# Performance work log

Measured on AMD Instinct MI355X. Metric: run time of the kernel, lower is better.

Reference implementation:

```python
import jax, jax.numpy as jnp
import numpy as np

B, HC, WC, KC = 4, 32, 32, 1024   # coarse feature map (ResNet101 layer3)
HF, WF, KF = 128, 128, 256        # fine feature map (ResNet101 layer1)
DC = 4                            # downscale_coef; HF // DC == HC


def setup_inputs() -> dict:
    key = jax.random.key(0)
    k1, k2, k3, k4 = jax.random.split(key, 4)
    return {
        "F_g1_coarse": jax.random.normal(k1, (B, HC, WC, KC), jnp.float32),
        "F_gk_coarse": jax.random.normal(k2, (B, HC, WC, KC), jnp.float32),
        "F_g1_fine": jax.random.normal(k3, (B, HF, WF, KF), jnp.float32),
        "F_gk_fine": jax.random.normal(k4, (B, HF, WF, KF), jnp.float32),
    }


def _coarse_match(f1, fk):
    # For every coarse position in Gk find nearest (L2) coarse position in G1.
    b, h, w, k = f1.shape
    a = f1.reshape(b, h * w, k)   # G1 positions
    q = fk.reshape(b, h * w, k)   # Gk positions
    # ||q||^2 + ||a||^2 - 2 q.a  -> [B, HW_gk, HW_g1]
    d = ((q * q).sum(-1)[:, :, None]
         + (a * a).sum(-1)[:, None, :]
         - 2.0 * jnp.einsum('bnk,bmk->bnm', q, a))
    idx = jnp.argmin(d, axis=-1)                       # [B, HW]
    cm = jnp.stack([idx // w, idx % w], axis=-1)       # (row, col) in G1
    return cm.reshape(b, h, w, 2).astype(jnp.int32)


def _fine_match(f1, fk, cm, dc):
    # Refine each dc x dc fine tile of Gk by searching the fine pixels of G1
    # covered by the coarse matches of the 3x3 coarse-neighborhood.
    b, h, w, k = fk.shape
    hc, wc = h // dc, w // dc
    off = jnp.arange(-1, 2)
    nI = jnp.clip(jnp.arange(hc)[:, None] + off[None, :], 0, hc - 1)  # [Hc,3]
    nJ = jnp.clip(jnp.arange(wc)[:, None] + off[None, :], 0, wc - 1)  # [Wc,3]
    # neighbor coarse matches: [B, Hc, Wc, 3, 3, 2]
    nb = cm[:, nI[:, None, :, None], nJ[None, :, None, :]]
    nb = nb.reshape(b, hc, wc, 9, 2)
    # expand each coarse match to its dc*dc fine pixels in G1
    sr = jnp.repeat(jnp.arange(dc), dc)   # [dc^2] row shifts
    sc = jnp.tile(jnp.arange(dc), dc)     # [dc^2] col shifts
    ncand = 9 * dc * dc                   # 144 candidates per tile
    cand_r = (nb[..., 0][..., None] * dc + sr).reshape(b, hc, wc, ncand)
    cand_c = (nb[..., 1][..., None] * dc + sc).reshape(b, hc, wc, ncand)
    # gather candidate fine features from G1: [B, Hc, Wc, N, K]
    bi = jnp.arange(b)[:, None, None, None]
    cand_f = f1[bi, cand_r, cand_c]
    # fine tile features of Gk: [B, Hc, Wc, dc^2, K]
    fkb = fk.reshape(b, hc, dc, wc, dc, k).transpose(0, 1, 3, 2, 4, 5)
    fkb = fkb.reshape(b, hc, wc, dc * dc, k)
    dist = ((fkb * fkb).sum(-1)[..., :, None]
            + (cand_f * cand_f).sum(-1)[..., None, :]
            - 2.0 * jnp.einsum('bhwpk,bhwnk->bhwpn', fkb, cand_f))
    best = jnp.argmin(dist, axis=-1)      # [B, Hc, Wc, dc^2]
    hi = jnp.arange(hc)[None, :, None, None]
    wi = jnp.arange(wc)[None, None, :, None]
    best_r = cand_r[bi, hi, wi, best]     # [B, Hc, Wc, dc^2]
    best_c = cand_c[bi, hi, wi, best]
    def to_grid(x):
        return x.reshape(b, hc, wc, dc, dc).transpose(0, 1, 3, 2, 4).reshape(b, h, w)
    return jnp.stack([to_grid(best_r), to_grid(best_c)], axis=-1).astype(jnp.int32)


def reference(F_g1_coarse, F_gk_coarse, F_g1_fine, F_gk_fine):
    closest_coarse = _coarse_match(F_g1_coarse, F_gk_coarse)   # [B,Hc,Wc,2]
    closest_fine = _fine_match(F_g1_fine, F_gk_fine, closest_coarse, DC)  # [B,H,W,2]
    return closest_coarse, closest_fine
```

## Files before the change

### kernel.cpp

```cpp
#include <hip/hip_runtime.h>
#include <cstdint>
#include <cstddef>

#define BB 4
#define HCC 32
#define WCC 32
#define KCC 1024
#define NCC (HCC*WCC)
#define HFF 128
#define WFF 128
#define KFF 256
#define DCC 4
#define NCHUNK 8

typedef _Float16 half8 __attribute__((ext_vector_type(8)));
typedef _Float16 half4_t __attribute__((ext_vector_type(4)));
typedef float f32x4 __attribute__((ext_vector_type(4)));
#define MFMA16(a,b,c) __builtin_amdgcn_mfma_f32_16x16x32_f16((a),(b),(c),0,0,0)
#define INV2K 0.00048828125f

__device__ inline void cvt8(const float4 u0, const float4 u1, half8& h, half8& l2) {
  float uu[8];
  *(float4*)uu = u0; *(float4*)(uu + 4) = u1;
  #pragma unroll
  for (int e = 0; e < 8; ++e) {
    _Float16 hh = (_Float16)uu[e];
    float r = (uu[e] - (float)hh) * 2048.0f;
    h[e] = hh; l2[e] = (_Float16)r;
  }
}

template<int K>
__global__ __launch_bounds__(256) void preconv_kernel(
    const float* __restrict__ src0, const float* __restrict__ src1,
    _Float16* __restrict__ hi0, _Float16* __restrict__ lo0,
    _Float16* __restrict__ hi1, _Float16* __restrict__ lo1,
    float* __restrict__ nr0, float* __restrict__ nr1, int rows) {
  const float* __restrict__ src = blockIdx.y ? src1 : src0;
  _Float16* __restrict__ hi = blockIdx.y ? hi1 : hi0;
  _Float16* __restrict__ lo = blockIdx.y ? lo1 : lo0;
  float* __restrict__ nrm = blockIdx.y ? nr1 : nr0;
  const int wave = threadIdx.x >> 6, lane = threadIdx.x & 63;
  const int row = blockIdx.x * 4 + wave;
  if (row >= rows) return;
  const float* p = src + (size_t)row * K;
  const size_t ob = (size_t)row * K + lane * 4;
  float s = 0.f;
  #pragma unroll
  for (int c = 0; c < K / 256; ++c) {
    float4 v = *(const float4*)(p + c * 256 + lane * 4);
    s += v.x*v.x + v.y*v.y + v.z*v.z + v.w*v.w;
    float vv[4] = {v.x, v.y, v.z, v.w};
    half4_t h, l2;
    #pragma unroll
    for (int e = 0; e < 4; ++e) {
      _Float16 hh = (_Float16)vv[e];
      l2[e] = (_Float16)((vv[e] - (float)hh) * 2048.0f);
      h[e] = hh;
    }
    *(half4_t*)(hi + ob + c * 256) = h;
    *(half4_t*)(lo + ob + c * 256) = l2;
  }
  #pragma unroll
  for (int m = 1; m <= 32; m <<= 1) s += __shfl_xor(s, m, 64);
  if (lane == 0) nrm[row] = s;
}

__global__ __launch_bounds__(256) void preconv_fine_kernel(
    const float* __restrict__ src, _Float16* __restrict__ hl,
    float* __restrict__ nrm, int rows) {
  const int wave = threadIdx.x >> 6, lane = threadIdx.x & 63;
  const int row = blockIdx.x * 4 + wave;
  if (row >= rows) return;
  float4 v = *(const float4*)(src + (size_t)row * KFF + lane * 4);
  float s = v.x*v.x + v.y*v.y + v.z*v.z + v.w*v.w;
  float vv[4] = {v.x, v.y, v.z, v.w};
  half4_t h, l2;
  #pragma unroll
  for (int e = 0; e < 4; ++e) {
    _Float16 hh = (_Float16)vv[e];
    l2[e] = (_Float16)((vv[e] - (float)hh) * 2048.0f);
    h[e] = hh;
  }
  const size_t dst = (size_t)row * 512 + (lane >> 3) * 64 + ((lane >> 1) & 3) * 16 + (lane & 1) * 4;
  *(half4_t*)(hl + dst)     = h;
  *(half4_t*)(hl + dst + 8) = l2;
  #pragma unroll
  for (int m = 1; m <= 32; m <<= 1) s += __shfl_xor(s, m, 64);
  if (lane == 0) nrm[row] = s;
}

__global__ __launch_bounds__(256) void coarse_kernel3(
    const _Float16* __restrict__ gAhi, const _Float16* __restrict__ gAlo,
    const _Float16* __restrict__ gBhi, const _Float16* __restrict__ gBlo,
    const float* __restrict__ na, const float* __restrict__ nq,
    float* __restrict__ pval, int* __restrict__ pidx) {
  __shared__ _Float16 Ahi[128][64], Alo[128][64];
  __shared__ _Float16 Bhi[64][64],  Blo[64][64];
  __shared__ float a2s[128], q2s[64];
  __shared__ float redv[2][64];
  __shared__ int   redi[2][64];

  const int t = threadIdx.x;
  const int chunk = blockIdx.x;
  const int n0 = blockIdx.y * 64;
  const int b  = blockIdx.z;
  const int m0 = chunk * 128;

  const int ar = t >> 1, ahf = t & 1;
  const int brw = t >> 2, bq = t & 3;
  const int l  = t & 63;
  const int wv = t >> 6;
  const int wm = wv >> 1, wn = wv & 1;

  if (t < 128) a2s[t] = na[b*NCC + m0 + t];
  else if (t < 192) q2s[t - 128] = nq[b*NCC + n0 + (t - 128)];

  const _Float16* __restrict__ gah = gAhi + (size_t)(b*NCC + m0 + ar) * KCC + ahf * 32;
  const _Float16* __restrict__ gal = gAlo + (size_t)(b*NCC + m0 + ar) * KCC + ahf * 32;
  const _Float16* __restrict__ gbh = gBhi + (size_t)(b*NCC + n0 + brw) * KCC + bq * 16;
  const _Float16* __restrict__ gbl = gBlo + (size_t)(b*NCC + n0 + brw) * KCC + bq * 16;

  f32x4 accA[4][2], accB[4][2];
  #pragma unroll
  for (int mt = 0; mt < 4; ++mt)
    #pragma unroll
    for (int nt = 0; nt < 2; ++nt) { accA[mt][nt] = (f32x4)0.f; accB[mt][nt] = (f32x4)0.f; }

  half8 pah[4], pal[4], pbh[2], pbl[2];
  #pragma unroll
  for (int c2 = 0; c2 < 4; ++c2) { pah[c2] = *(const half8*)(gah + c2*8); pal[c2] = *(const half8*)(gal + c2*8); }
  #pragma unroll
  for (int c2 = 0; c2 < 2; ++c2) { pbh[c2] = *(const half8*)(gbh + c2*8); pbl[c2] = *(const half8*)(gbl + c2*8); }

  for (int k0 = 0; k0 < KCC; k0 += 64) {
    __syncthreads();
    #pragma unroll
    for (int c2 = 0; c2 < 4; ++c2) {
      int cs = (ahf * 4 + c2) ^ (ar & 7);
      *(half8*)&Ahi[ar][cs * 8] = pah[c2];
      *(half8*)&Alo[ar][cs * 8] = pal[c2];
    }
    #pragma unroll
    for (int c2 = 0; c2 < 2; ++c2) {
      int cs = (bq * 2 + c2) ^ (brw & 7);
      *(half8*)&Bhi[brw][cs * 8] = pbh[c2];
      *(half8*)&Blo[brw][cs * 8] = pbl[c2];
    }
    __syncthreads();

    if (k0 + 64 < KCC) {
      #pragma unroll
      for (int c2 = 0; c2 < 4; ++c2) {
        pah[c2] = *(const half8*)(gah + k0 + 64 + c2*8);
        pal[c2] = *(const half8*)(gal + k0 + 64 + c2*8);
      }
      #pragma unroll
      for (int c2 = 0; c2 < 2; ++c2) {
        pbh[c2] = *(const half8*)(gbh + k0 + 64 + c2*8);
        pbl[c2] = *(const half8*)(gbl + k0 + 64 + c2*8);
      }
    }

    #pragma unroll
    for (int kk = 0; kk < 2; ++kk) {
      const int cs = ((kk * 4 + (l >> 4)) ^ (l & 7)) * 8;
      half8 ah[4], al[4], bh[2], bl[2];
      #pragma unroll
      for (int mt = 0; mt < 4; ++mt) {
        int row = wm * 64 + mt * 16 + (l & 15);
        ah[mt] = *(const half8*)&Ahi[row][cs];
        al[mt] = *(const half8*)&Alo[row][cs];
      }
      #pragma unroll
      for (int nt = 0; nt < 2; ++nt) {
        int row = wn * 32 + nt * 16 + (l & 15);
        bh[nt] = *(const half8*)&Bhi[row][cs];
        bl[nt] = *(const half8*)&Blo[row][cs];
      }
      #pragma unroll
      for (int mt = 0; mt < 4; ++mt)
        #pragma unroll
        for (int nt = 0; nt < 2; ++nt) {
          accA[mt][nt] = MFMA16(ah[mt], bh[nt], accA[mt][nt]);
          accB[mt][nt] = MFMA16(ah[mt], bl[nt], accB[mt][nt]);
          accB[mt][nt] = MFMA16(al[mt], bh[nt], accB[mt][nt]);
        }
    }
  }

  #pragma unroll
  for (int nt = 0; nt < 2; ++nt) {
    float q2 = q2s[wn * 32 + nt * 16 + (l & 15)];
    float bv = 3.0e38f; int bi = 0;
    #pragma unroll
    for (int mt = 0; mt < 4; ++mt)
      #pragma unroll
      for (int r = 0; r < 4; ++r) {
        float dot = accA[mt][nt][r] + accB[mt][nt][r] * INV2K;
        int ml = wm * 64 + mt * 16 + (l >> 4) * 4 + r;
        float d = (q2 + a2s[ml]) - 2.0f * dot;
        if (d < bv) { bv = d; bi = m0 + ml; }
      }
    #pragma unroll
    for (int mm = 16; mm < 64; mm <<= 1) {
      float ov = __shfl_xor(bv, mm, 64);
      int oi = __shfl_xor(bi, mm, 64);
      if (ov < bv || (ov == bv && oi < bi)) { bv = ov; bi = oi; }
    }
    if ((l >> 4) == 0) { redv[wm][wn*32 + nt*16 + l] = bv; redi[wm][wn*32 + nt*16 + l] = bi; }
  }
  __syncthreads();
  if (t < 64) {
    float v0 = redv[0][t]; int i0 = redi[0][t];
    float v1 = redv[1][t]; int i1 = redi[1][t];
    if (v1 < v0) { v0 = v1; i0 = i1; }
    pval[((size_t)b * NCC + n0 + t) * NCHUNK + chunk] = v0;
    pidx[((size_t)b * NCC + n0 + t) * NCHUNK + chunk] = i0;
  }
}

__global__ __launch_bounds__(256) void coarse_reduce_kernel(
    const float* __restrict__ pval, const int* __restrict__ pidx,
    int* __restrict__ out) {
  int g = blockIdx.x * 256 + threadIdx.x;
  if (g >= BB * NCC) return;
  float bv = pval[(size_t)g * NCHUNK];
  int bi = pidx[(size_t)g * NCHUNK];
  #pragma unroll
  for (int c = 1; c < NCHUNK; ++c) {
    float v = pval[(size_t)g * NCHUNK + c];
    int ix = pidx[(size_t)g * NCHUNK + c];
    if (v < bv) { bv = v; bi = ix; }
  }
  out[(size_t)g*2]     = bi >> 5;
  out[(size_t)g*2 + 1] = bi & 31;
}

__global__ __launch_bounds__(512, 2) void fine_kernel6(
    const _Float16* __restrict__ gHL, const float* __restrict__ fkf,
    const float* __restrict__ naf, const int* __restrict__ coarse,
    int* __restrict__ outf) {
  __shared__ _Float16 CS[2][384 * 64];
  __shared__ int   rIdx[384];
  __shared__ float tNORM[384];
  __shared__ int cbr[24], cbc[24];
  __shared__ float redv[8][16];
  __shared__ int   redi[8][16];

  const int t = threadIdx.x;
  const int bx = blockIdx.x, by = blockIdx.y, b = blockIdx.z;
  const int l = t & 63, w = t >> 6;
  const int cy = w >> 2, cx = w & 3;
  const int ii = by * 2 + cy, jj = bx * 4 + cx;

  if (t < 24) {
    int wy = t / 6, wx = t % 6;
    int y = min(max(by * 2 - 1 + wy, 0), HCC - 1);
    int x = min(max(bx * 4 - 1 + wx, 0), WCC - 1);
    int base = ((b * HCC + y) * WCC + x) * 2;
    cbr[t] = coarse[base]; cbc[t] = coarse[base + 1];
  }
  __syncthreads();
  if (t < 384) {
    int slot = t >> 4, s = t & 15;
    int row = cbr[slot] * DCC + (s >> 2), col = cbc[slot] * DCC + (s & 3);
    int g = (b * HFF + row) * WFF + col;
    rIdx[t] = g; tNORM[t] = naf[g];
  }
  __syncthreads();

  unsigned srcOff[6], dstOff[6];
  #pragma unroll
  for (int it = 0; it < 6; ++it) {
    int g2 = it * 512 + t;
    int rowG = g2 >> 3, lc = g2 & 7;
    srcOff[it] = (unsigned)rIdx[rowG] * 512u + (unsigned)((lc >> 1) * 16 + (lc & 1) * 8);
    dstOff[it] = (unsigned)(rowG * 64 + (lc ^ (rowG & 7)) * 8);
  }

  const int q = l >> 4, r = l & 15;
  const int qfr = ii * DCC + (r >> 2), qfc = jj * DCC + (r & 3);
  const float* qsrc = fkf + ((size_t)(b * HFF + qfr) * WFF + qfc) * KFF + q * 8;

  half8 pf[6];
  #pragma unroll
  for (int it = 0; it < 6; ++it) pf[it] = *(const half8*)(gHL + srcOff[it]);
  #pragma unroll
  for (int it = 0; it < 6; ++it) *(half8*)&CS[0][dstOff[it]] = pf[it];
  #pragma unroll
  for (int it = 0; it < 6; ++it) pf[it] = *(const half8*)(gHL + srcOff[it] + 64u);
  float4 qu0 = *(const float4*)(qsrc);
  float4 qu1 = *(const float4*)(qsrc + 4);
  __syncthreads();

  f32x4 accA[9], accB[9];
  #pragma unroll
  for (int T = 0; T < 9; ++T) { accA[T] = (f32x4)0.f; accB[T] = (f32x4)0.f; }

  const int woff[9] = {0, 1, 2, 6, 7, 8, 12, 13, 14};
  const int wbase = cy * 6 + cx;
  const int rsw = r & 7;
  const int c0 = ((q * 2) ^ rsw) * 8, c1 = ((q * 2 + 1) ^ rsw) * 8;
  float qnp = 0.f;

  #pragma unroll
  for (int ke = 0; ke < 8; ++ke) {
    const int cur = ke & 1;
    qnp += qu0.x*qu0.x + qu0.y*qu0.y + qu0.z*qu0.z + qu0.w*qu0.w
         + qu1.x*qu1.x + qu1.y*qu1.y + qu1.z*qu1.z + qu1.w*qu1.w;
    half8 bh, bl;
    cvt8(qu0, qu1, bh, bl);
    if (ke < 7) {
      qu0 = *(const float4*)(qsrc + (ke + 1) * 32);
      qu1 = *(const float4*)(qsrc + (ke + 1) * 32 + 4);
    }
    #pragma unroll
    for (int T = 0; T < 9; ++T) {
      int rowG = (wbase + woff[T]) * 16 + r;
      half8 ah = *(const half8*)&CS[cur][rowG * 64 + c0];
      half8 al = *(const half8*)&CS[cur][rowG * 64 + c1];
      accA[T] = MFMA16(ah, bh, accA[T]);
      accB[T] = MFMA16(ah, bl, accB[T]);
      accB[T] = MFMA16(al, bh, accB[T]);
    }
    if (ke < 7) {
      #pragma unroll
      for (int it = 0; it < 6; ++it) *(half8*)&CS[cur ^ 1][dstOff[it]] = pf[it];
      if (ke < 6) {
        #pragma unroll
        for (int it = 0; it < 6; ++it)
          pf[it] = *(const half8*)(gHL + srcOff[it] + (unsigned)(ke + 2) * 64u);
      }
    }
    __syncthreads();
  }

  qnp += __shfl_xor(qnp, 16, 64);
  qnp += __shfl_xor(qnp, 32, 64);
  const float q2v = qnp;

  {
    float bv = 3.0e38f; int bi = 0;
    #pragma unroll
    for (int T = 0; T < 9; ++T) {
      int slot = wbase + woff[T];
      #pragma unroll
      for (int r2 = 0; r2 < 4; ++r2) {
        int s4 = q * 4 + r2;
        float cn = tNORM[slot * 16 + s4];
        float dot = accA[T][r2] + accB[T][r2] * INV2K;
        float d = (q2v + cn) - 2.0f * dot;
        int m = T * 16 + s4;
        if (d < bv) { bv = d; bi = m; }
      }
    }
    #pragma unroll
    for (int mm = 16; mm < 64; mm <<= 1) {
      float ov = __shfl_xor(bv, mm, 64);
      int oi = __shfl_xor(bi, mm, 64);
      if (ov < bv || (ov == bv && oi < bi)) { bv = ov; bi = oi; }
    }
    if (l < 16) {
      int T = bi >> 4, s3 = bi & 15, slot = wbase + woff[T];
      int br = cbr[slot] * DCC + (s3 >> 2);
      int bc = cbc[slot] * DCC + (s3 & 3);
      int fr = ii * DCC + (l >> 2), fc = jj * DCC + (l & 3);
      size_t ob = ((size_t)(b * HFF + fr) * WFF + fc) * 2;
      outf[ob]     = br;
      outf[ob + 1] = bc;
    }
  }
  (void)redv; (void)redi;
}

__global__ __launch_bounds__(256, 2) void coarse_kernel(
    const float* __restrict__ f1, const float* __restrict__ fk,
    float* __restrict__ pval, int* __restrict__ pidx) {
  __shared__ _Float16 Ahi[128][64], Alo[128][64];
  __shared__ _Float16 Bhi[64][64],  Blo[64][64];
  __shared__ float npA[256], npB[256];
  __shared__ float a2s[128], q2s[64];
  __shared__ float redv[2][64];
  __shared__ int   redi[2][64];

  const int t = threadIdx.x;
  const int chunk = blockIdx.x;
  const int n0 = blockIdx.y * 64;
  const int b  = blockIdx.z;
  const int m0 = chunk * 128;

  const float* __restrict__ Abase = f1 + ((size_t)b * NCC + m0) * KCC;
  const float* __restrict__ Bbase = fk + ((size_t)b * NCC + n0) * KCC;

  const int ar = t >> 1, ahf = t & 1;
  const int brw = t >> 2, bq = t & 3;
  const int l  = t & 63;
  const int wv = t >> 6;
  const int wm = wv >> 1, wn = wv & 1;

  float nrmA = 0.f, nrmB = 0.f;
  f32x4 accA[4][2], accB[4][2];
  #pragma unroll
  for (int mt = 0; mt < 4; ++mt)
    #pragma unroll
    for (int nt = 0; nt < 2; ++nt) { accA[mt][nt] = (f32x4)0.f; accB[mt][nt] = (f32x4)0.f; }

  for (int k0 = 0; k0 < KCC; k0 += 64) {
    __syncthreads();
    {
      const float4* src = (const float4*)(Abase + (size_t)ar * KCC + k0 + ahf * 32);
      float4 va[8];
      #pragma unroll
      for (int i2 = 0; i2 < 8; ++i2) va[i2] = src[i2];
      #pragma unroll
      for (int i2 = 0; i2 < 8; ++i2)
        nrmA += va[i2].x*va[i2].x + va[i2].y*va[i2].y + va[i2].z*va[i2].z + va[i2].w*va[i2].w;
      #pragma unroll
      for (int c2 = 0; c2 < 4; ++c2) {
        half8 hh, hl;
        cvt8(va[c2*2], va[c2*2+1], hh, hl);
        int cs = (ahf * 4 + c2) ^ (ar & 7);
        *(half8*)&Ahi[ar][cs * 8] = hh;
        *(half8*)&Alo[ar][cs * 8] = hl;
      }
    }
    {
      const float4* src = (const float4*)(Bbase + (size_t)brw * KCC + k0 + bq * 16);
      float4 vb[4];
      #pragma unroll
      for (int i2 = 0; i2 < 4; ++i2) vb[i2] = src[i2];
      #pragma unroll
      for (int i2 = 0; i2 < 4; ++i2)
        nrmB += vb[i2].x*vb[i2].x + vb[i2].y*vb[i2].y + vb[i2].z*vb[i2].z + vb[i2].w*vb[i2].w;
      #pragma unroll
      for (int c2 = 0; c2 < 2; ++c2) {
        half8 hh, hl;
        cvt8(vb[c2*2], vb[c2*2+1], hh, hl);
        int cs = (bq * 2 + c2) ^ (brw & 7);
        *(half8*)&Bhi[brw][cs * 8] = hh;
        *(half8*)&Blo[brw][cs * 8] = hl;
      }
    }
    __syncthreads();

    #pragma unroll
    for (int kk = 0; kk < 2; ++kk) {
      const int cs = ((kk * 4 + (l >> 4)) ^ (l & 7)) * 8;
      half8 ah[4], al[4], bh[2], bl[2];
      #pragma unroll
      for (int mt = 0; mt < 4; ++mt) {
        int row = wm * 64 + mt * 16 + (l & 15);
        ah[mt] = *(const half8*)&Ahi[row][cs];
        al[mt] = *(const half8*)&Alo[row][cs];
      }
      #pragma unroll
      for (int nt = 0; nt < 2; ++nt) {
        int row = wn * 32 + nt * 16 + (l & 15);
        bh[nt] = *(const half8*)&Bhi[row][cs];
        bl[nt] = *(const half8*)&Blo[row][cs];
      }
      #pragma unroll
      for (int mt = 0; mt < 4; ++mt)
        #pragma unroll
        for (int nt = 0; nt < 2; ++nt) {
          accA[mt][nt] = MFMA16(ah[mt], bh[nt], accA[mt][nt]);
          accB[mt][nt] = MFMA16(ah[mt], bl[nt], accB[mt][nt]);
          accB[mt][nt] = MFMA16(al[mt], bh[nt], accB[mt][nt]);
        }
    }
  }

  npA[t] = nrmA; npB[t] = nrmB;
  __syncthreads();
  if (t < 128) a2s[t] = npA[2*t] + npA[2*t + 1];
  if (t < 64)  q2s[t] = npB[4*t] + npB[4*t + 1] + npB[4*t + 2] + npB[4*t + 3];
  __syncthreads();

  #pragma unroll
  for (int nt = 0; nt < 2; ++nt) {
    float q2 = q2s[wn * 32 + nt * 16 + (l & 15)];
    float bv = 3.0e38f; int bi = 0;
    #pragma unroll
    for (int mt = 0; mt < 4; ++mt)
      #pragma unroll
      for (int r = 0; r < 4; ++r) {
        float dot = accA[mt][nt][r] + accB[mt][nt][r] * INV2K;
        int ml = wm * 64 + mt * 16 + (l >> 4) * 4 + r;
        float d = (q2 + a2s[ml]) - 2.0f * dot;
        if (d < bv) { bv = d; bi = m0 + ml; }
      }
    #pragma unroll
    for (int mm = 16; mm < 64; mm <<= 1) {
      float ov = __shfl_xor(bv, mm, 64);
      int oi = __shfl_xor(bi, mm, 64);
      if (ov < bv || (ov == bv && oi < bi)) { bv = ov; bi = oi; }
    }
    if ((l >> 4) == 0) { redv[wm][wn*32 + nt*16 + l] = bv; redi[wm][wn*32 + nt*16 + l] = bi; }
  }
  __syncthreads();
  if (t < 64) {
    float v0 = redv[0][t]; int i0 = redi[0][t];
    float v1 = redv[1][t]; int i1 = redi[1][t];
    if (v1 < v0) { v0 = v1; i0 = i1; }
    pval[((size_t)b * NCC + n0 + t) * NCHUNK + chunk] = v0;
    pidx[((size_t)b * NCC + n0 + t) * NCHUNK + chunk] = i0;
  }
}

__global__ __launch_bounds__(192) void fine_kernel(
    const float* __restrict__ f1, const float* __restrict__ fkf,
    const int* __restrict__ coarse, int* __restrict__ outf) {
  __shared__ _Float16 Qhi[16][256], Qlo[16][256];
  __shared__ float qn[16], cn[144];
  __shared__ int cROW[144];
  __shared__ int cbr[9], cbc[9];
  __shared__ float redv[3][16];
  __shared__ int   redi[3][16];

  const int t = threadIdx.x;
  const int j = blockIdx.x, i = blockIdx.y, b = blockIdx.z;
  const int l = t & 63, wv = t >> 6;

  if (t < 9) {
    int di = t / 3 - 1, dj = t % 3 - 1;
    int y = min(max(i + di, 0), HCC - 1);
    int x = min(max(j + dj, 0), WCC - 1);
    int base = ((b*HCC + y)*WCC + x) * 2;
    cbr[t] = coarse[base];
    cbc[t] = coarse[base + 1];
  }
  __syncthreads();
  if (t < 144) {
    int n9 = t >> 4, s = t & 15;
    int row = cbr[n9]*DCC + (s >> 2), col = cbc[n9]*DCC + (s & 3);
    cROW[t] = (b*HFF + row)*WFF + col;
  }
  if (t < 64) {
    int qr = l & 15, qq = l >> 4;
    int fr = i*DCC + (qr >> 2), fc = j*DCC + (qr & 3);
    const float* src = fkf + ((size_t)(b*HFF + fr)*WFF + fc) * KFF + qq * 64;
    float s2 = 0.f;
    #pragma unroll
    for (int c2 = 0; c2 < 8; ++c2) {
      float4 u0 = *(const float4*)(src + c2*8);
      float4 u1 = *(const float4*)(src + c2*8 + 4);
      s2 += u0.x*u0.x + u0.y*u0.y + u0.z*u0.z + u0.w*u0.w
          + u1.x*u1.x + u1.y*u1.y + u1.z*u1.z + u1.w*u1.w;
      half8 hh, hl;
      cvt8(u0, u1, hh, hl);
      int cs = (qq * 8 + c2) ^ (qr & 7);
      *(half8*)&Qhi[qr][cs * 8] = hh;
      *(half8*)&Qlo[qr][cs * 8] = hl;
    }
    s2 += __shfl_xor(s2, 16, 64);
    s2 += __shfl_xor(s2, 32, 64);
    if (qq == 0) qn[qr] = s2;
  }
  __syncthreads();

  const float* ap[3];
  #pragma unroll
  for (int T = 0; T < 3; ++T)
    ap[T] = f1 + (size_t)cROW[(wv*3 + T)*16 + (l & 15)] * KFF;

  f32x4 accA[3], accB[3];
  float nrmp[3];
  #pragma unroll
  for (int T = 0; T < 3; ++T) { accA[T] = (f32x4)0.f; accB[T] = (f32x4)0.f; nrmp[T] = 0.f; }

  #pragma unroll 2
  for (int s = 0; s < 8; ++s) {
    const int cs = ((s * 4 + (l >> 4)) ^ (l & 7)) * 8;
    half8 bh = *(const half8*)&Qhi[l & 15][cs];
    half8 bl = *(const half8*)&Qlo[l & 15][cs];
    #pragma unroll
    for (int T = 0; T < 3; ++T) {
      const float* p = ap[T] + s*32 + (l >> 4)*8;
      float4 u0 = *(const float4*)p;
      float4 u1 = *(const float4*)(p + 4);
      nrmp[T] += u0.x*u0.x + u0.y*u0.y + u0.z*u0.z + u0.w*u0.w
               + u1.x*u1.x + u1.y*u1.y + u1.z*u1.z + u1.w*u1.w;
      half8 ahv, alv;
      cvt8(u0, u1, ahv, alv);
      accA[T] = MFMA16(ahv, bh, accA[T]);
      accB[T] = MFMA16(ahv, bl, accB[T]);
      accB[T] = MFMA16(alv, bh, accB[T]);
    }
  }

  #pragma unroll
  for (int T = 0; T < 3; ++T) {
    float np = nrmp[T];
    np += __shfl_xor(np, 16, 64);
    np += __shfl_xor(np, 32, 64);
    if ((l >> 4) == 0) cn[(wv*3 + T)*16 + l] = np;
  }
  __syncthreads();

  {
    float q2 = qn[l & 15];
    float bv = 3.0e38f; int bi = 0;
    #pragma unroll
    for (int T = 0; T < 3; ++T)
      #pragma unroll
      for (int r = 0; r < 4; ++r) {
        float dot = accA[T][r] + accB[T][r] * INV2K;
        int m = (wv*3 + T)*16 + (l >> 4)*4 + r;
        float d = (q2 + cn[m]) - 2.0f * dot;
        if (d < bv) { bv = d; bi = m; }
      }
    #pragma unroll
    for (int mm = 16; mm < 64; mm <<= 1) {
      float ov = __shfl_xor(bv, mm, 64);
      int oi = __shfl_xor(bi, mm, 64);
      if (ov < bv || (ov == bv && oi < bi)) { bv = ov; bi = oi; }
    }
    if ((l >> 4) == 0 && l < 16) { redv[wv][l] = bv; redi[wv][l] = bi; }
  }
  __syncthreads();

  if (t < 16) {
    float v = redv[0][t]; int ix = redi[0][t];
    #pragma unroll
    for (int w = 1; w < 3; ++w) {
      float ov = redv[w][t];
      if (ov < v) { v = ov; ix = redi[w][t]; }
    }
    int n9 = ix >> 4, s3 = ix & 15;
    int br = cbr[n9]*DCC + (s3 >> 2);
    int bc = cbc[n9]*DCC + (s3 & 3);
    int fr = i*DCC + (t >> 2), fc = j*DCC + (t & 3);
    size_t ob = ((size_t)(b*HFF + fr)*WFF + fc) * 2;
    outf[ob]     = br;
    outf[ob + 1] = bc;
  }
}

extern "C" void kernel_launch(void* const* d_in, const int* in_sizes, int n_in,
                              void* d_out, int out_size, void* d_ws, size_t ws_size,
                              hipStream_t stream) {
  (void)in_sizes; (void)n_in; (void)out_size;
  const float* f1c = (const float*)d_in[0];
  const float* fkc = (const float*)d_in[1];
  const float* f1f = (const float*)d_in[2];
  const float* fkf = (const float*)d_in[3];
  int* out = (int*)d_out;

  const size_t NEED = 101220352;
  if (ws_size >= NEED) {
    char* w = (char*)d_ws;
    _Float16* cAhi = (_Float16*)(w);
    _Float16* cAlo = (_Float16*)(w + 8388608);
    _Float16* cBhi = (_Float16*)(w + 16777216);
    _Float16* cBlo = (_Float16*)(w + 25165824);
    _Float16* fHL  = (_Float16*)(w + 33554432);
    float* na_c = (float*)(w + 100663296);
    float* nq_c = (float*)(w + 100679680);
    float* na_f = (float*)(w + 100696064);
    float* pval = (float*)(w + 100958208);
    int*   pidx = (int*)  (w + 101089280);

    preconv_kernel<KCC><<<dim3(BB*NCC/4, 2), 256, 0, stream>>>(
        f1c, fkc, cAhi, cAlo, cBhi, cBlo, na_c, nq_c, BB*NCC);
    preconv_fine_kernel<<<dim3(BB*HFF*WFF/4), 256, 0, stream>>>(
        f1f, fHL, na_f, BB*HFF*WFF);
    coarse_kernel3<<<dim3(NCHUNK, NCC/64, BB), 256, 0, stream>>>(
        cAhi, cAlo, cBhi, cBlo, na_c, nq_c, pval, pidx);
    coarse_reduce_kernel<<<dim3((BB*NCC + 255)/256), 256, 0, stream>>>(pval, pidx, out);
    fine_kernel6<<<dim3(WCC/4, HCC/2, BB), 512, 0, stream>>>(
        fHL, fkf, na_f, out, out + BB*NCC*2);
  } else {
    float* pval = (float*)d_ws;
    int*   pidx = (int*)((float*)d_ws + BB*NCC*NCHUNK);
    coarse_kernel<<<dim3(NCHUNK, NCC/64, BB), 256, 0, stream>>>(f1c, fkc, pval, pidx);
    coarse_reduce_kernel<<<dim3((BB*NCC + 255)/256), 256, 0, stream>>>(pval, pidx, out);
    fine_kernel<<<dim3(WCC, HCC, BB), 192, 0, stream>>>(f1f, fkf, out, out + BB*NCC*2);
  }
}
```

Measured before the change: 104.9 us.

## Enlarge coarse GEMM and fine-match tiles to 128x128 and 4x4 per block

The coarse distance kernel moves from 64-query by 128-candidate tiles with 256 threads to 128x128 tiles with 512 threads (8 waves in a 2x4 layout). This halves the number of blocks and reuses each staged A tile across twice as many queries. The fine kernel grows from a 2x4 to a 4x4 coarse-cell block with 1024 threads, so overlapping candidate neighbourhoods share one shared-memory staging (576 candidate rows instead of 384). In exchange, the larger tiles use more shared memory and allow fewer resident blocks, and the fine kernel now has a ragged final load iteration that needs predication.

Result: slower. 194.2 us (+85.2%).

```diff
diff --git a/kernel.cpp b/kernel.cpp
--- a/kernel.cpp
+++ b/kernel.cpp
@@ -90,36 +90,35 @@
   if (lane == 0) nrm[row] = s;
 }
 
-__global__ __launch_bounds__(256) void coarse_kernel3(
+__global__ __launch_bounds__(512) void coarse_kernel4(
     const _Float16* __restrict__ gAhi, const _Float16* __restrict__ gAlo,
     const _Float16* __restrict__ gBhi, const _Float16* __restrict__ gBlo,
     const float* __restrict__ na, const float* __restrict__ nq,
     float* __restrict__ pval, int* __restrict__ pidx) {
   __shared__ _Float16 Ahi[128][64], Alo[128][64];
-  __shared__ _Float16 Bhi[64][64],  Blo[64][64];
-  __shared__ float a2s[128], q2s[64];
-  __shared__ float redv[2][64];
-  __shared__ int   redi[2][64];
+  __shared__ _Float16 Bhi[128][64], Blo[128][64];
+  __shared__ float a2s[128], q2s[128];
+  __shared__ float redv[2][128];
+  __shared__ int   redi[2][128];
 
   const int t = threadIdx.x;
-  const int chunk = blockIdx.x;
-  const int n0 = blockIdx.y * 64;
+  const int n0 = blockIdx.x * 128;
+  const int chunk = blockIdx.y;
   const int b  = blockIdx.z;
   const int m0 = chunk * 128;
 
-  const int ar = t >> 1, ahf = t & 1;
-  const int brw = t >> 2, bq = t & 3;
+  const int row = t >> 2, q4 = t & 3;
   const int l  = t & 63;
   const int wv = t >> 6;
-  const int wm = wv >> 1, wn = wv & 1;
+  const int wm = wv >> 2, wn = wv & 3;
 
   if (t < 128) a2s[t] = na[b*NCC + m0 + t];
-  else if (t < 192) q2s[t - 128] = nq[b*NCC + n0 + (t - 128)];
-
-  const _Float16* __restrict__ gah = gAhi + (size_t)(b*NCC + m0 + ar) * KCC + ahf * 32;
-  const _Float16* __restrict__ gal = gAlo + (size_t)(b*NCC + m0 + ar) * KCC + ahf * 32;
-  const _Float16* __restrict__ gbh = gBhi + (size_t)(b*NCC + n0 + brw) * KCC + bq * 16;
-  const _Float16* __restrict__ gbl = gBlo + (size_t)(b*NCC + n0 + brw) * KCC + bq * 16;
+  else if (t < 256) q2s[t - 128] = nq[b*NCC + n0 + (t - 128)];
+
+  const _Float16* __restrict__ gah = gAhi + (size_t)(b*NCC + m0 + row) * KCC + q4 * 16;
+  const _Float16* __restrict__ gal = gAlo + (size_t)(b*NCC + m0 + row) * KCC + q4 * 16;
+  const _Float16* __restrict__ gbh = gBhi + (size_t)(b*NCC + n0 + row) * KCC + q4 * 16;
+  const _Float16* __restrict__ gbl = gBlo + (size_t)(b*NCC + n0 + row) * KCC + q4 * 16;
 
   f32x4 accA[4][2], accB[4][2];
   #pragma unroll
@@ -127,38 +126,32 @@
     #pragma unroll
     for (int nt = 0; nt < 2; ++nt) { accA[mt][nt] = (f32x4)0.f; accB[mt][nt] = (f32x4)0.f; }
 
-  half8 pah[4], pal[4], pbh[2], pbl[2];
-  #pragma unroll
-  for (int c2 = 0; c2 < 4; ++c2) { pah[c2] = *(const half8*)(gah + c2*8); pal[c2] = *(const half8*)(gal + c2*8); }
-  #pragma unroll
-  for (int c2 = 0; c2 < 2; ++c2) { pbh[c2] = *(const half8*)(gbh + c2*8); pbl[c2] = *(const half8*)(gbl + c2*8); }
+  half8 pah[2], pal[2], pbh[2], pbl[2];
+  #pragma unroll
+  for (int c = 0; c < 2; ++c) {
+    pah[c] = *(const half8*)(gah + c*8); pal[c] = *(const half8*)(gal + c*8);
+    pbh[c] = *(const half8*)(gbh + c*8); pbl[c] = *(const half8*)(gbl + c*8);
+  }
 
   for (int k0 = 0; k0 < KCC; k0 += 64) {
     __syncthreads();
     #pragma unroll
-    for (int c2 = 0; c2 < 4; ++c2) {
-      int cs = (ahf * 4 + c2) ^ (ar & 7);
-      *(half8*)&Ahi[ar][cs * 8] = pah[c2];
-      *(half8*)&Alo[ar][cs * 8] = pal[c2];
-    }
-    #pragma unroll
-    for (int c2 = 0; c2 < 2; ++c2) {
-      int cs = (bq * 2 + c2) ^ (brw & 7);
-      *(half8*)&Bhi[brw][cs * 8] = pbh[c2];
-      *(half8*)&Blo[brw][cs * 8] = pbl[c2];
+    for (int c = 0; c < 2; ++c) {
+      int cs = (q4 * 2 + c) ^ (row & 7);
+      *(half8*)&Ahi[row][cs * 8] = pah[c];
+      *(half8*)&Alo[row][cs * 8] = pal[c];
+      *(half8*)&Bhi[row][cs * 8] = pbh[c];
+      *(half8*)&Blo[row][cs * 8] = pbl[c];
     }
     __syncthreads();
 
     if (k0 + 64 < KCC) {
       #pragma unroll
-      for (int c2 = 0; c2 < 4; ++c2) {
-        pah[c2] = *(const half8*)(gah + k0 + 64 + c2*8);
-        pal[c2] = *(const half8*)(gal + k0 + 64 + c2*8);
-      }
-      #pragma unroll
-      for (int c2 = 0; c2 < 2; ++c2) {
-        pbh[c2] = *(const half8*)(gbh + k0 + 64 + c2*8);
-        pbl[c2] = *(const half8*)(gbl + k0 + 64 + c2*8);
+      for (int c = 0; c < 2; ++c) {
+        pah[c] = *(const half8*)(gah + k0 + 64 + c*8);
+        pal[c] = *(const half8*)(gal + k0 + 64 + c*8);
+        pbh[c] = *(const half8*)(gbh + k0 + 64 + c*8);
+        pbl[c] = *(const half8*)(gbl + k0 + 64 + c*8);
       }
     }
 
@@ -168,15 +161,15 @@
       half8 ah[4], al[4], bh[2], bl[2];
       #pragma unroll
       for (int mt = 0; mt < 4; ++mt) {
-        int row = wm * 64 + mt * 16 + (l & 15);
-        ah[mt] = *(const half8*)&Ahi[row][cs];
-        al[mt] = *(const half8*)&Alo[row][cs];
+        int rw = wm * 64 + mt * 16 + (l & 15);
+        ah[mt] = *(const half8*)&Ahi[rw][cs];
+        al[mt] = *(const half8*)&Alo[rw][cs];
       }
       #pragma unroll
       for (int nt = 0; nt < 2; ++nt) {
-        int row = wn * 32 + nt * 16 + (l & 15);
-        bh[nt] = *(const half8*)&Bhi[row][cs];
-        bl[nt] = *(const half8*)&Blo[row][cs];
+        int rw = wn * 32 + nt * 16 + (l & 15);
+        bh[nt] = *(const half8*)&Bhi[rw][cs];
+        bl[nt] = *(const half8*)&Blo[rw][cs];
       }
       #pragma unroll
       for (int mt = 0; mt < 4; ++mt)
@@ -211,7 +204,7 @@
     if ((l >> 4) == 0) { redv[wm][wn*32 + nt*16 + l] = bv; redi[wm][wn*32 + nt*16 + l] = bi; }
   }
   __syncthreads();
-  if (t < 64) {
+  if (t < 128) {
     float v0 = redv[0][t]; int i0 = redi[0][t];
     float v1 = redv[1][t]; int i1 = redi[1][t];
     if (v1 < v0) { v0 = v1; i0 = i1; }
@@ -237,32 +230,30 @@
   out[(size_t)g*2 + 1] = bi & 31;
 }
 
-__global__ __launch_bounds__(512, 2) void fine_kernel6(
+__global__ __launch_bounds__(1024) void fine_kernel7(
     const _Float16* __restrict__ gHL, const float* __restrict__ fkf,
     const float* __restrict__ naf, const int* __restrict__ coarse,
     int* __restrict__ outf) {
-  __shared__ _Float16 CS[2][384 * 64];
-  __shared__ int   rIdx[384];
-  __shared__ float tNORM[384];
-  __shared__ int cbr[24], cbc[24];
-  __shared__ float redv[8][16];
-  __shared__ int   redi[8][16];
+  __shared__ _Float16 CS[2][576 * 64];
+  __shared__ int   rIdx[576];
+  __shared__ float tNORM[576];
+  __shared__ int cbr[36], cbc[36];
 
   const int t = threadIdx.x;
   const int bx = blockIdx.x, by = blockIdx.y, b = blockIdx.z;
   const int l = t & 63, w = t >> 6;
   const int cy = w >> 2, cx = w & 3;
-  const int ii = by * 2 + cy, jj = bx * 4 + cx;
-
-  if (t < 24) {
+  const int ii = by * 4 + cy, jj = bx * 4 + cx;
+
+  if (t < 36) {
     int wy = t / 6, wx = t % 6;
-    int y = min(max(by * 2 - 1 + wy, 0), HCC - 1);
+    int y = min(max(by * 4 - 1 + wy, 0), HCC - 1);
     int x = min(max(bx * 4 - 1 + wx, 0), WCC - 1);
     int base = ((b * HCC + y) * WCC + x) * 2;
     cbr[t] = coarse[base]; cbc[t] = coarse[base + 1];
   }
   __syncthreads();
-  if (t < 384) {
+  if (t < 576) {
     int slot = t >> 4, s = t & 15;
     int row = cbr[slot] * DCC + (s >> 2), col = cbc[slot] * DCC + (s & 3);
     int g = (b * HFF + row) * WFF + col;
@@ -270,26 +261,31 @@
   }
   __syncthreads();
 
-  unsigned srcOff[6], dstOff[6];
-  #pragma unroll
-  for (int it = 0; it < 6; ++it) {
-    int g2 = it * 512 + t;
-    int rowG = g2 >> 3, lc = g2 & 7;
+  unsigned srcOff[5], dstOff[5];
+  #pragma unroll
+  for (int it = 0; it < 5; ++it) {
+    int g2 = it * 1024 + t;
+    int g3 = (g2 < 4608) ? g2 : 0;
+    int rowG = g3 >> 3, lc = g3 & 7;
     srcOff[it] = (unsigned)rIdx[rowG] * 512u + (unsigned)((lc >> 1) * 16 + (lc & 1) * 8);
     dstOff[it] = (unsigned)(rowG * 64 + (lc ^ (rowG & 7)) * 8);
   }
+  const bool vLast = (t < 4608 - 4 * 1024);
 
   const int q = l >> 4, r = l & 15;
   const int qfr = ii * DCC + (r >> 2), qfc = jj * DCC + (r & 3);
   const float* qsrc = fkf + ((size_t)(b * HFF + qfr) * WFF + qfc) * KFF + q * 8;
 
-  half8 pf[6];
-  #pragma unroll
-  for (int it = 0; it < 6; ++it) pf[it] = *(const half8*)(gHL + srcOff[it]);
-  #pragma unroll
-  for (int it = 0; it < 6; ++it) *(half8*)&CS[0][dstOff[it]] = pf[it];
-  #pragma unroll
-  for (int it = 0; it < 6; ++it) pf[it] = *(const half8*)(gHL + srcOff[it] + 64u);
+  half8 pf[5];
+  #pragma unroll
+  for (int it = 0; it < 4; ++it) pf[it] = *(const half8*)(gHL + srcOff[it]);
+  if (vLast) pf[4] = *(const half8*)(gHL + srcOff[4]);
+  #pragma unroll
+  for (int it = 0; it < 4; ++it) *(half8*)&CS[0][dstOff[it]] = pf[it];
+  if (vLast) *(half8*)&CS[0][dstOff[4]] = pf[4];
+  #pragma unroll
+  for (int it = 0; it < 4; ++it) pf[it] = *(const half8*)(gHL + srcOff[it] + 64u);
+  if (vLast) pf[4] = *(const half8*)(gHL + srcOff[4] + 64u);
   float4 qu0 = *(const float4*)(qsrc);
   float4 qu1 = *(const float4*)(qsrc + 4);
   __syncthreads();
@@ -326,11 +322,13 @@
     }
     if (ke < 7) {
       #pragma unroll
-      for (int it = 0; it < 6; ++it) *(half8*)&CS[cur ^ 1][dstOff[it]] = pf[it];
+      for (int it = 0; it < 4; ++it) *(half8*)&CS[cur ^ 1][dstOff[it]] = pf[it];
+      if (vLast) *(half8*)&CS[cur ^ 1][dstOff[4]] = pf[4];
       if (ke < 6) {
         #pragma unroll
-        for (int it = 0; it < 6; ++it)
+        for (int it = 0; it < 4; ++it)
           pf[it] = *(const half8*)(gHL + srcOff[it] + (unsigned)(ke + 2) * 64u);
+        if (vLast) pf[4] = *(const half8*)(gHL + srcOff[4] + (unsigned)(ke + 2) * 64u);
       }
     }
     __syncthreads();
@@ -371,7 +369,6 @@
       outf[ob + 1] = bc;
     }
   }
-  (void)redv; (void)redi;
 }
 
 __global__ __launch_bounds__(256, 2) void coarse_kernel(
@@ -450,15 +447,15 @@
       half8 ah[4], al[4], bh[2], bl[2];
       #pragma unroll
       for (int mt = 0; mt < 4; ++mt) {
-        int row = wm * 64 + mt * 16 + (l & 15);
-        ah[mt] = *(const half8*)&Ahi[row][cs];
-        al[mt] = *(const half8*)&Alo[row][cs];
+        int rw = wm * 64 + mt * 16 + (l & 15);
+        ah[mt] = *(const half8*)&Ahi[rw][cs];
+        al[mt] = *(const half8*)&Alo[rw][cs];
       }
       #pragma unroll
       for (int nt = 0; nt < 2; ++nt) {
-        int row = wn * 32 + nt * 16 + (l & 15);
-        bh[nt] = *(const half8*)&Bhi[row][cs];
-        bl[nt] = *(const half8*)&Blo[row][cs];
+        int rw = wn * 32 + nt * 16 + (l & 15);
+        bh[nt] = *(const half8*)&Bhi[rw][cs];
+        bl[nt] = *(const half8*)&Blo[rw][cs];
       }
       #pragma unroll
       for (int mt = 0; mt < 4; ++mt)
@@ -665,10 +662,10 @@
         f1c, fkc, cAhi, cAlo, cBhi, cBlo, na_c, nq_c, BB*NCC);
     preconv_fine_kernel<<<dim3(BB*HFF*WFF/4), 256, 0, stream>>>(
         f1f, fHL, na_f, BB*HFF*WFF);
-    coarse_kernel3<<<dim3(NCHUNK, NCC/64, BB), 256, 0, stream>>>(
+    coarse_kernel4<<<dim3(NCC/128, NCC/128, BB), 512, 0, stream>>>(
         cAhi, cAlo, cBhi, cBlo, na_c, nq_c, pval, pidx);
     coarse_reduce_kernel<<<dim3((BB*NCC + 255)/256), 256, 0, stream>>>(pval, pidx, out);
-    fine_kernel6<<<dim3(WCC/4, HCC/2, BB), 512, 0, stream>>>(
+    fine_kernel7<<<dim3(WCC/4, HCC/4, BB), 1024, 0, stream>>>(
         fHL, fkf, na_f, out, out + BB*NCC*2);
   } else {
     float* pval = (float*)d_ws;
```
